# Optimization experiments

Measured on AMD Instinct MI355X. Metric: run time of the kernel, lower is better.

## Reference

```python
import jax, jax.numpy as jnp
import numpy as np


def setup_inputs() -> dict:
    key = jax.random.key(0)
    k_x, k_m, k_w1, k_b1, k_w2, k_b2 = jax.random.split(key, 6)
    b, seq_len, d_in, d_out = 8, 4096, 1024, 512
    x = jax.random.normal(k_x, (b, seq_len, d_in), dtype=jnp.float32)
    # binary-ish mask in {0,1} as floats (torch code multiplies by mask)
    mask = (jax.random.uniform(k_m, (b, seq_len)) < 0.5).astype(jnp.float32)
    s1 = 1.0 / np.sqrt(d_in)
    s2 = 1.0 / np.sqrt(d_out)
    W_enc = jax.random.uniform(k_w1, (d_out, d_in), minval=-s1, maxval=s1, dtype=jnp.float32)
    b_enc = jax.random.uniform(k_b1, (d_out,), minval=-s1, maxval=s1, dtype=jnp.float32)
    W_dec = jax.random.uniform(k_w2, (d_in, d_out), minval=-s2, maxval=s2, dtype=jnp.float32)
    b_dec = jax.random.uniform(k_b2, (d_in,), minval=-s2, maxval=s2, dtype=jnp.float32)
    return {"x": x, "mask": mask, "W_enc": W_enc, "b_enc": b_enc, "W_dec": W_dec, "b_dec": b_dec}


def reference(x, mask, W_enc, b_enc, W_dec, b_dec):
    # per-step: v_t = v_{t-1} + relu(x_t @ W_enc^T + b_enc) * mask_t  -> additive scan == cumsum
    h = jax.nn.relu(jnp.einsum('bsd,od->bso', x, W_enc) + b_enc) * mask[:, :, None]  # [b,s,d_out]
    v_cum = jnp.cumsum(h, axis=1)  # [b,s,d_out]
    out_enc = jnp.einsum('bso,do->bsd', v_cum, W_dec) + b_dec  # decode every prefix state
    v = v_cum[:, -1, :]  # final accumulated state
    return (v, out_enc)
```

## Files before the change

kernel.cpp:

```cpp
#include <hip/hip_runtime.h>
#include <hip/hip_bf16.h>
#include <stdint.h>

typedef __bf16 bf16_t;
typedef __bf16 bf16x4 __attribute__((ext_vector_type(4)));
typedef __bf16 bf16x8 __attribute__((ext_vector_type(8)));
typedef float  f32x4  __attribute__((ext_vector_type(4)));

__device__ __forceinline__ void gload_lds16(const void* g, void* l) {
  __builtin_amdgcn_global_load_lds(
      (__attribute__((address_space(1))) void*)g,
      (__attribute__((address_space(3))) void*)l, 16, 0, 0);
}

__global__ void cast_weights(const float* __restrict__ a, bf16_t* __restrict__ oa,
                             const float* __restrict__ b, bf16_t* __restrict__ ob,
                             int n4each) {
  const int i = blockIdx.x * blockDim.x + threadIdx.x;
  const float* src;
  bf16_t* dst;
  int k;
  if (i < n4each) { src = a; dst = oa; k = i; }
  else            { src = b; dst = ob; k = i - n4each; }
  f32x4 v = reinterpret_cast<const f32x4*>(src)[k];
  bf16x4 o;
  o[0] = (bf16_t)v[0]; o[1] = (bf16_t)v[1]; o[2] = (bf16_t)v[2]; o[3] = (bf16_t)v[3];
  reinterpret_cast<bf16x4*>(dst)[k] = o;
}

__global__ __launch_bounds__(256) void gemm1_fused(
    const float* __restrict__ x, const bf16_t* __restrict__ Wenc,
    const float* __restrict__ b_enc, const float* __restrict__ mask,
    bf16_t* __restrict__ h, float* __restrict__ partials)
{
  __shared__ __align__(16) char smem[65536];
  bf16_t* As0 = (bf16_t*)(smem);
  bf16_t* As1 = (bf16_t*)(smem + 16384);
  bf16_t* Bs0 = (bf16_t*)(smem + 32768);
  bf16_t* Bs1 = (bf16_t*)(smem + 49152);
  float*  tile = (float*)smem;

  const int tid  = threadIdx.x;
  const int lane = tid & 63;
  const int w    = tid >> 6;
  const int wm   = w >> 1, wn = w & 1;
  const long bm  = (long)blockIdx.x * 128;
  const long bn  = (long)blockIdx.y * 128;

  f32x4 acc[4][4] = {};

  const int srow = w * 32 + (lane >> 3);
  const int scol = (lane & 7) * 8;
  const bf16_t* Bbase = Wenc + (bn + srow) * 1024 + scol;

  const int ar0 = tid >> 3;
  const int ac0 = (tid & 7) * 8;
  const float* Abase = x + (bm + ar0) * 1024 + ac0;

  f32x4 av[4][2];

  auto aload = [&](int kt) {
    #pragma unroll
    for (int p = 0; p < 4; ++p) {
      const float* s = Abase + (long)p * 32 * 1024 + kt;
      av[p][0] = *reinterpret_cast<const f32x4*>(s);
      av[p][1] = *reinterpret_cast<const f32x4*>(s + 4);
    }
  };
  auto awrite = [&](bf16_t* As) {
    #pragma unroll
    for (int p = 0; p < 4; ++p) {
      bf16x8 o;
      #pragma unroll
      for (int e = 0; e < 4; ++e) {
        o[e]     = (bf16_t)av[p][0][e];
        o[e + 4] = (bf16_t)av[p][1][e];
      }
      *reinterpret_cast<bf16x8*>(&As[(p * 32 + ar0) * 64 + ac0]) = o;
    }
  };
  auto bstage = [&](bf16_t* Bs, int kt) {
    #pragma unroll
    for (int it = 0; it < 4; ++it)
      gload_lds16(Bbase + (long)it * 8 * 1024 + kt, &Bs[(w * 32 + it * 8) * 64]);
  };
  auto mfma_tile = [&](const bf16_t* As, const bf16_t* Bs) {
    #pragma unroll
    for (int kk = 0; kk < 2; ++kk) {
      const int kof = kk * 32 + (lane >> 4) * 8;
      bf16x8 afr[4], bfr[4];
      #pragma unroll
      for (int i = 0; i < 4; ++i)
        afr[i] = *reinterpret_cast<const bf16x8*>(&As[(wm * 64 + i * 16 + (lane & 15)) * 64 + kof]);
      #pragma unroll
      for (int j = 0; j < 4; ++j)
        bfr[j] = *reinterpret_cast<const bf16x8*>(&Bs[(wn * 64 + j * 16 + (lane & 15)) * 64 + kof]);
      #pragma unroll
      for (int i = 0; i < 4; ++i)
        #pragma unroll
        for (int j = 0; j < 4; ++j)
          acc[i][j] = __builtin_amdgcn_mfma_f32_16x16x32_bf16(afr[i], bfr[j], acc[i][j], 0, 0, 0);
    }
  };

  aload(0);
  awrite(As0);
  bstage(Bs0, 0);
  __syncthreads();

  int kt = 64;
  for (int p2 = 0; p2 < 8; ++p2) {
    if (kt < 1024) { aload(kt); bstage(Bs1, kt); }
    mfma_tile(As0, Bs0);
    if (kt < 1024) awrite(As1);
    __syncthreads();
    kt += 64;

    if (kt < 1024) { aload(kt); bstage(Bs0, kt); }
    mfma_tile(As1, Bs1);
    if (kt < 1024) awrite(As0);
    __syncthreads();
    kt += 64;
  }

  float bv[4];
  #pragma unroll
  for (int j = 0; j < 4; ++j)
    bv[j] = b_enc[bn + wn * 64 + j * 16 + (lane & 15)];

  #pragma unroll
  for (int i = 0; i < 4; ++i) {
    const int rbase = wm * 64 + i * 16 + ((lane >> 4) << 2);
    const f32x4 mv = *reinterpret_cast<const f32x4*>(&mask[bm + rbase]);
    #pragma unroll
    for (int j = 0; j < 4; ++j) {
      const int colj = wn * 64 + j * 16 + (lane & 15);
      #pragma unroll
      for (int r = 0; r < 4; ++r) {
        const int row = rbase + r;
        float hv = acc[i][j][r] + bv[j];
        hv = hv > 0.f ? hv : 0.f;
        hv *= mv[r];
        tile[row * 128 + (colj ^ (((row >> 2) & 1) << 4))] = hv;
      }
    }
  }
  __syncthreads();

  if (tid < 128) {
    float run = 0.f;
    bf16_t* hp = h + bm * 512 + bn + tid;
    #pragma unroll 4
    for (int s = 0; s < 128; ++s) {
      run += tile[s * 128 + (tid ^ (((s >> 2) & 1) << 4))];
      hp[(long)s * 512] = (bf16_t)run;
    }
    partials[blockIdx.x * 512 + bn + tid] = run;
  }
}

template<int EPI>
__global__ __launch_bounds__(256) void gemm_bt(
    const bf16_t* __restrict__ A, const bf16_t* __restrict__ B,
    const int K, const int N,
    const float* __restrict__ bias,
    const float* __restrict__ Padd,
    float* __restrict__ outf)
{
  __shared__ __align__(16) bf16_t As[2][128 * 64];
  __shared__ __align__(16) bf16_t Bs[2][128 * 64];

  const int tid  = threadIdx.x;
  const int lane = tid & 63;
  const int w    = tid >> 6;
  const int wm   = w >> 1, wn = w & 1;
  const long bm  = (long)blockIdx.x * 128;
  const long bn  = (long)blockIdx.y * 128;

  f32x4 acc[4][4] = {};

  const int srow = w * 32 + (lane >> 3);
  const int scol = (lane & 7) * 8;
  const bf16_t* Abase = A + (bm + srow) * (long)K + scol;
  const bf16_t* Bbase = B + (bn + srow) * (long)K + scol;

  auto stageA = [&](bf16_t* dst, int kt) {
    #pragma unroll
    for (int it = 0; it < 4; ++it)
      gload_lds16(Abase + (long)it * 8 * K + kt, &dst[(w * 32 + it * 8) * 64]);
  };
  auto stageB = [&](bf16_t* dst, int kt) {
    #pragma unroll
    for (int it = 0; it < 4; ++it)
      gload_lds16(Bbase + (long)it * 8 * K + kt, &dst[(w * 32 + it * 8) * 64]);
  };
  auto mfma_tile = [&](const bf16_t* Asb, const bf16_t* Bsb) {
    #pragma unroll
    for (int kk = 0; kk < 2; ++kk) {
      const int kof = kk * 32 + (lane >> 4) * 8;
      bf16x8 afr[4], bfr[4];
      #pragma unroll
      for (int i = 0; i < 4; ++i)
        afr[i] = *reinterpret_cast<const bf16x8*>(&Asb[(wm * 64 + i * 16 + (lane & 15)) * 64 + kof]);
      #pragma unroll
      for (int j = 0; j < 4; ++j)
        bfr[j] = *reinterpret_cast<const bf16x8*>(&Bsb[(wn * 64 + j * 16 + (lane & 15)) * 64 + kof]);
      #pragma unroll
      for (int i = 0; i < 4; ++i)
        #pragma unroll
        for (int j = 0; j < 4; ++j)
          acc[i][j] = __builtin_amdgcn_mfma_f32_16x16x32_bf16(afr[i], bfr[j], acc[i][j], 0, 0, 0);
    }
  };

  stageA(As[0], 0);
  stageB(Bs[0], 0);
  __syncthreads();

  int kt = 64;
  const int NP = K >> 7;
  for (int p2 = 0; p2 < NP; ++p2) {
    if (kt < K) { stageA(As[1], kt); stageB(Bs[1], kt); }
    mfma_tile(As[0], Bs[0]);
    __syncthreads();
    kt += 64;

    if (kt < K) { stageA(As[0], kt); stageB(Bs[0], kt); }
    mfma_tile(As[1], Bs[1]);
    __syncthreads();
    kt += 64;
  }

  #pragma unroll
  for (int j = 0; j < 4; ++j) {
    const long gc = bn + wn * 64 + j * 16 + (lane & 15);
    const float addv = (EPI == 1) ? Padd[(bm >> 7) * (long)N + gc] : bias[gc];
    #pragma unroll
    for (int i = 0; i < 4; ++i) {
      const long gr0 = bm + wm * 64 + i * 16 + ((lane >> 4) << 2);
      #pragma unroll
      for (int r = 0; r < 4; ++r)
        outf[(gr0 + r) * (long)N + gc] = acc[i][j][r] + addv;
    }
  }
}

__global__ void scan_chunks(const float* __restrict__ partials, bf16_t* __restrict__ prefixb,
                            float* __restrict__ v_out) {
  const int idx = blockIdx.x * blockDim.x + threadIdx.x;
  const int b = idx >> 9;
  const int o = idx & 511;
  float run = 0.f;
  #pragma unroll
  for (int c = 0; c < 32; ++c) {
    const size_t off = ((size_t)(b * 32 + c)) * 512 + o;
    prefixb[off] = (bf16_t)run;
    run += partials[off];
  }
  v_out[idx] = run;
}

extern "C" void kernel_launch(void* const* d_in, const int* in_sizes, int n_in,
                              void* d_out, int out_size, void* d_ws, size_t ws_size,
                              hipStream_t stream) {
  const float* x     = (const float*)d_in[0];
  const float* mask  = (const float*)d_in[1];
  const float* W_enc = (const float*)d_in[2];
  const float* b_enc = (const float*)d_in[3];
  const float* W_dec = (const float*)d_in[4];
  const float* b_dec = (const float*)d_in[5];

  float* out     = (float*)d_out;
  float* v_out   = out;
  float* out_enc = out + 4096;

  char* ws = (char*)d_ws;
  bf16_t* Web      = (bf16_t*)ws;  ws += (size_t)512 * 1024 * 2;
  bf16_t* Wdb      = (bf16_t*)ws;  ws += (size_t)1024 * 512 * 2;
  bf16_t* h        = (bf16_t*)ws;  ws += (size_t)32768 * 512 * 2;
  float*  partials = (float*)ws;   ws += (size_t)256 * 512 * 4;
  bf16_t* prefixb  = (bf16_t*)ws;  ws += (size_t)256 * 512 * 2;
  float*  P        = (float*)ws;   ws += (size_t)256 * 1024 * 4;

  cast_weights<<<1024, 256, 0, stream>>>(W_enc, Web, W_dec, Wdb, 131072);

  gemm1_fused<<<dim3(256, 4), 256, 0, stream>>>(x, Web, b_enc, mask, h, partials);

  scan_chunks<<<16, 256, 0, stream>>>(partials, prefixb, v_out);

  gemm_bt<2><<<dim3(2, 8), 256, 0, stream>>>(prefixb, Wdb, 512, 1024, b_dec, nullptr, P);

  gemm_bt<1><<<dim3(256, 8), 256, 0, stream>>>(h, Wdb, 512, 1024, nullptr, P, out_enc);
}
```

Before: 165.2 us.

## XOR-swizzle LDS tiles in both GEMMs and parallelize the in-block scan

Adds an XOR swizzle to the LDS layouts of the A and B tiles in the encoder and decoder GEMMs. The x tile is now loaded row-coalesced as float4 and written swizzled, which is meant to remove LDS bank conflicts on the MFMA fragment reads. The epilogue tile is stored in bf16 with a row-wise swizzle, and the 128-row cumsum is split across all 256 threads using a two-half partial sum instead of 128 serial threads. An explicit vmcnt(0) wait before each barrier adds a stall, and rounding h to bf16 before the scan slightly changes numerics.

```diff
diff --git a/kernel.cpp b/kernel.cpp
--- a/kernel.cpp
+++ b/kernel.cpp
@@ -17,9 +17,7 @@
                              const float* __restrict__ b, bf16_t* __restrict__ ob,
                              int n4each) {
   const int i = blockIdx.x * blockDim.x + threadIdx.x;
-  const float* src;
-  bf16_t* dst;
-  int k;
+  const float* src; bf16_t* dst; int k;
   if (i < n4each) { src = a; dst = oa; k = i; }
   else            { src = b; dst = ob; k = i - n4each; }
   f32x4 v = reinterpret_cast<const f32x4*>(src)[k];
@@ -28,17 +26,14 @@
   reinterpret_cast<bf16x4*>(dst)[k] = o;
 }
 
-__global__ __launch_bounds__(256) void gemm1_fused(
+__global__ __launch_bounds__(256) void gemm1_128(
     const float* __restrict__ x, const bf16_t* __restrict__ Wenc,
     const float* __restrict__ b_enc, const float* __restrict__ mask,
-    bf16_t* __restrict__ h, float* __restrict__ partials)
+    bf16_t* __restrict__ h_out, float* __restrict__ partials)
 {
   __shared__ __align__(16) char smem[65536];
-  bf16_t* As0 = (bf16_t*)(smem);
-  bf16_t* As1 = (bf16_t*)(smem + 16384);
-  bf16_t* Bs0 = (bf16_t*)(smem + 32768);
-  bf16_t* Bs1 = (bf16_t*)(smem + 49152);
-  float*  tile = (float*)smem;
+  auto Al = [&](int buf) { return (bf16_t*)(smem + buf * 16384); };
+  auto Bl = [&](int buf) { return (bf16_t*)(smem + 32768 + buf * 16384); };
 
   const int tid  = threadIdx.x;
   const int lane = tid & 63;
@@ -46,55 +41,52 @@
   const int wm   = w >> 1, wn = w & 1;
   const long bm  = (long)blockIdx.x * 128;
   const long bn  = (long)blockIdx.y * 128;
+  const int NT   = 16;
 
   f32x4 acc[4][4] = {};
-
-  const int srow = w * 32 + (lane >> 3);
-  const int scol = (lane & 7) * 8;
-  const bf16_t* Bbase = Wenc + (bn + srow) * 1024 + scol;
-
-  const int ar0 = tid >> 3;
-  const int ac0 = (tid & 7) * 8;
-  const float* Abase = x + (bm + ar0) * 1024 + ac0;
-
-  f32x4 av[4][2];
-
-  auto aload = [&](int kt) {
-    #pragma unroll
-    for (int p = 0; p < 4; ++p) {
-      const float* s = Abase + (long)p * 32 * 1024 + kt;
-      av[p][0] = *reinterpret_cast<const f32x4*>(s);
-      av[p][1] = *reinterpret_cast<const f32x4*>(s + 4);
-    }
-  };
-  auto awrite = [&](bf16_t* As) {
-    #pragma unroll
-    for (int p = 0; p < 4; ++p) {
-      bf16x8 o;
-      #pragma unroll
-      for (int e = 0; e < 4; ++e) {
-        o[e]     = (bf16_t)av[p][0][e];
-        o[e + 4] = (bf16_t)av[p][1][e];
-      }
-      *reinterpret_cast<bf16x8*>(&As[(p * 32 + ar0) * 64 + ac0]) = o;
-    }
-  };
-  auto bstage = [&](bf16_t* Bs, int kt) {
-    #pragma unroll
-    for (int it = 0; it < 4; ++it)
-      gload_lds16(Bbase + (long)it * 8 * 1024 + kt, &Bs[(w * 32 + it * 8) * 64]);
-  };
-  auto mfma_tile = [&](const bf16_t* As, const bf16_t* Bs) {
+  f32x4 av[8];
+
+  auto gaLoad = [&](int t) {
+    #pragma unroll
+    for (int u = 0; u < 8; ++u) {
+      const int row = u * 16 + (tid >> 4);
+      av[u] = *reinterpret_cast<const f32x4*>(x + (bm + row) * 1024 + t * 64 + (tid & 15) * 4);
+    }
+  };
+  auto aWrite = [&](int buf) {
+    bf16_t* lb = Al(buf);
+    const int c4 = tid & 15;
+    #pragma unroll
+    for (int u = 0; u < 8; ++u) {
+      const int row = u * 16 + (tid >> 4);
+      bf16x4 o;
+      o[0] = (bf16_t)av[u][0]; o[1] = (bf16_t)av[u][1];
+      o[2] = (bf16_t)av[u][2]; o[3] = (bf16_t)av[u][3];
+      *reinterpret_cast<bf16x4*>(lb + row * 64 + ((((c4 >> 1) ^ (row & 7)) << 3) + (c4 & 1) * 4)) = o;
+    }
+  };
+  const int scolB = (((lane & 7) ^ (lane >> 3)) << 3);
+  auto stageB = [&](int t, int buf) {
+    bf16_t* lb = Bl(buf);
+    #pragma unroll
+    for (int it = 0; it < 4; ++it) {
+      const int r0 = w * 32 + it * 8;
+      gload_lds16(Wenc + (bn + r0 + (lane >> 3)) * 1024 + t * 64 + scolB, lb + r0 * 64);
+    }
+  };
+  auto mfma_tile = [&](int buf) {
+    const bf16_t* Asb = Al(buf);
+    const bf16_t* Bsb = Bl(buf);
     #pragma unroll
     for (int kk = 0; kk < 2; ++kk) {
-      const int kof = kk * 32 + (lane >> 4) * 8;
+      const int kof = (((kk * 4 + (lane >> 4)) ^ (lane & 7)) << 3);
       bf16x8 afr[4], bfr[4];
       #pragma unroll
       for (int i = 0; i < 4; ++i)
-        afr[i] = *reinterpret_cast<const bf16x8*>(&As[(wm * 64 + i * 16 + (lane & 15)) * 64 + kof]);
+        afr[i] = *reinterpret_cast<const bf16x8*>(&Asb[(wm * 64 + i * 16 + (lane & 15)) * 64 + kof]);
       #pragma unroll
       for (int j = 0; j < 4; ++j)
-        bfr[j] = *reinterpret_cast<const bf16x8*>(&Bs[(wn * 64 + j * 16 + (lane & 15)) * 64 + kof]);
+        bfr[j] = *reinterpret_cast<const bf16x8*>(&Bsb[(wn * 64 + j * 16 + (lane & 15)) * 64 + kof]);
       #pragma unroll
       for (int i = 0; i < 4; ++i)
         #pragma unroll
@@ -103,26 +95,22 @@
     }
   };
 
-  aload(0);
-  awrite(As0);
-  bstage(Bs0, 0);
-  __syncthreads();
-
-  int kt = 64;
-  for (int p2 = 0; p2 < 8; ++p2) {
-    if (kt < 1024) { aload(kt); bstage(Bs1, kt); }
-    mfma_tile(As0, Bs0);
-    if (kt < 1024) awrite(As1);
+  gaLoad(0);
+  stageB(0, 0);
+  aWrite(0);
+  asm volatile("s_waitcnt vmcnt(0)" ::: "memory");
+  __syncthreads();
+
+  for (int t = 0; t < NT; ++t) {
+    const int buf = t & 1;
+    if (t + 1 < NT) { gaLoad(t + 1); stageB(t + 1, buf ^ 1); }
+    mfma_tile(buf);
+    if (t + 1 < NT) aWrite(buf ^ 1);
+    asm volatile("s_waitcnt vmcnt(0)" ::: "memory");
     __syncthreads();
-    kt += 64;
-
-    if (kt < 1024) { aload(kt); bstage(Bs0, kt); }
-    mfma_tile(As1, Bs1);
-    if (kt < 1024) awrite(As0);
-    __syncthreads();
-    kt += 64;
-  }
-
+  }
+
+  bf16_t* tile = (bf16_t*)smem;
   float bv[4];
   #pragma unroll
   for (int j = 0; j < 4; ++j)
@@ -130,40 +118,50 @@
 
   #pragma unroll
   for (int i = 0; i < 4; ++i) {
-    const int rbase = wm * 64 + i * 16 + ((lane >> 4) << 2);
-    const f32x4 mv = *reinterpret_cast<const f32x4*>(&mask[bm + rbase]);
+    const int row0 = wm * 64 + i * 16 + ((lane >> 4) << 2);
+    const f32x4 mv = *reinterpret_cast<const f32x4*>(&mask[bm + row0]);
     #pragma unroll
     for (int j = 0; j < 4; ++j) {
-      const int colj = wn * 64 + j * 16 + (lane & 15);
-      #pragma unroll
-      for (int r = 0; r < 4; ++r) {
-        const int row = rbase + r;
-        float hv = acc[i][j][r] + bv[j];
-        hv = hv > 0.f ? hv : 0.f;
-        hv *= mv[r];
-        tile[row * 128 + (colj ^ (((row >> 2) & 1) << 4))] = hv;
+      const int col = wn * 64 + j * 16 + (lane & 15);
+      #pragma unroll
+      for (int e = 0; e < 4; ++e) {
+        const int row = row0 + e;
+        float hv = acc[i][j][e] + bv[j];
+        hv = (hv > 0.f ? hv : 0.f) * mv[e];
+        tile[row * 128 + (col ^ ((row & 7) << 4))] = (bf16_t)hv;
       }
     }
   }
   __syncthreads();
 
-  if (tid < 128) {
-    float run = 0.f;
-    bf16_t* hp = h + bm * 512 + bn + tid;
+  __shared__ float sum0[128];
+  const int col  = tid & 127;
+  const int half = tid >> 7;
+  if (half == 0) {
+    float s = 0.f;
     #pragma unroll 4
-    for (int s = 0; s < 128; ++s) {
-      run += tile[s * 128 + (tid ^ (((s >> 2) & 1) << 4))];
-      hp[(long)s * 512] = (bf16_t)run;
-    }
-    partials[blockIdx.x * 512 + bn + tid] = run;
-  }
-}
-
-template<int EPI>
-__global__ __launch_bounds__(256) void gemm_bt(
+    for (int r = 0; r < 64; ++r)
+      s += (float)tile[r * 128 + (col ^ ((r & 7) << 4))];
+    sum0[col] = s;
+  }
+  __syncthreads();
+  {
+    float run = half ? sum0[col] : 0.f;
+    const int rbase = half * 64;
+    bf16_t* hp = h_out + (bm + rbase) * 512 + bn + col;
+    #pragma unroll 4
+    for (int r = 0; r < 64; ++r) {
+      const int row = rbase + r;
+      run += (float)tile[row * 128 + (col ^ ((row & 7) << 4))];
+      hp[(long)r * 512] = (bf16_t)run;
+    }
+    if (half) partials[blockIdx.x * 512 + bn + col] = run;
+  }
+}
+
+__global__ __launch_bounds__(256) void gemm2_128(
     const bf16_t* __restrict__ A, const bf16_t* __restrict__ B,
     const int K, const int N,
-    const float* __restrict__ bias,
     const float* __restrict__ Padd,
     float* __restrict__ outf)
 {
@@ -176,6 +174,78 @@
   const int wm   = w >> 1, wn = w & 1;
   const long bm  = (long)blockIdx.x * 128;
   const long bn  = (long)blockIdx.y * 128;
+  const int NT   = K >> 6;
+
+  f32x4 acc[4][4] = {};
+
+  const int scol = (((lane & 7) ^ (lane >> 3)) << 3);
+  auto stage = [&](int t, int buf) {
+    #pragma unroll
+    for (int it = 0; it < 4; ++it) {
+      const int r0 = w * 32 + it * 8;
+      gload_lds16(A + (bm + r0 + (lane >> 3)) * (long)K + t * 64 + scol, &As[buf][r0 * 64]);
+      gload_lds16(B + (bn + r0 + (lane >> 3)) * (long)K + t * 64 + scol, &Bs[buf][r0 * 64]);
+    }
+  };
+  auto mfma_tile = [&](int buf) {
+    #pragma unroll
+    for (int kk = 0; kk < 2; ++kk) {
+      const int kof = (((kk * 4 + (lane >> 4)) ^ (lane & 7)) << 3);
+      bf16x8 afr[4], bfr[4];
+      #pragma unroll
+      for (int i = 0; i < 4; ++i)
+        afr[i] = *reinterpret_cast<const bf16x8*>(&As[buf][(wm * 64 + i * 16 + (lane & 15)) * 64 + kof]);
+      #pragma unroll
+      for (int j = 0; j < 4; ++j)
+        bfr[j] = *reinterpret_cast<const bf16x8*>(&Bs[buf][(wn * 64 + j * 16 + (lane & 15)) * 64 + kof]);
+      #pragma unroll
+      for (int i = 0; i < 4; ++i)
+        #pragma unroll
+        for (int j = 0; j < 4; ++j)
+          acc[i][j] = __builtin_amdgcn_mfma_f32_16x16x32_bf16(afr[i], bfr[j], acc[i][j], 0, 0, 0);
+    }
+  };
+
+  stage(0, 0);
+  asm volatile("s_waitcnt vmcnt(0)" ::: "memory");
+  __syncthreads();
+  for (int t = 0; t < NT; ++t) {
+    const int buf = t & 1;
+    if (t + 1 < NT) stage(t + 1, buf ^ 1);
+    mfma_tile(buf);
+    asm volatile("s_waitcnt vmcnt(0)" ::: "memory");
+    __syncthreads();
+  }
+
+  #pragma unroll
+  for (int j = 0; j < 4; ++j) {
+    const long gc = bn + wn * 64 + j * 16 + (lane & 15);
+    const float pv = Padd[blockIdx.x * (long)N + gc];
+    #pragma unroll
+    for (int i = 0; i < 4; ++i) {
+      const long gr0 = bm + wm * 64 + i * 16 + ((lane >> 4) << 2);
+      #pragma unroll
+      for (int e = 0; e < 4; ++e)
+        outf[(gr0 + e) * (long)N + gc] = acc[i][j][e] + pv;
+    }
+  }
+}
+
+__global__ __launch_bounds__(256) void gemm_p(
+    const bf16_t* __restrict__ A, const bf16_t* __restrict__ B,
+    const int K, const int N,
+    const float* __restrict__ bias,
+    float* __restrict__ outf)
+{
+  __shared__ __align__(16) bf16_t As[2][128 * 64];
+  __shared__ __align__(16) bf16_t Bs[2][128 * 64];
+
+  const int tid  = threadIdx.x;
+  const int lane = tid & 63;
+  const int w    = tid >> 6;
+  const int wm   = w >> 1, wn = w & 1;
+  const long bm  = (long)blockIdx.x * 128;
+  const long bn  = (long)blockIdx.y * 128;
 
   f32x4 acc[4][4] = {};
 
@@ -184,15 +254,12 @@
   const bf16_t* Abase = A + (bm + srow) * (long)K + scol;
   const bf16_t* Bbase = B + (bn + srow) * (long)K + scol;
 
-  auto stageA = [&](bf16_t* dst, int kt) {
-    #pragma unroll
-    for (int it = 0; it < 4; ++it)
-      gload_lds16(Abase + (long)it * 8 * K + kt, &dst[(w * 32 + it * 8) * 64]);
-  };
-  auto stageB = [&](bf16_t* dst, int kt) {
-    #pragma unroll
-    for (int it = 0; it < 4; ++it)
-      gload_lds16(Bbase + (long)it * 8 * K + kt, &dst[(w * 32 + it * 8) * 64]);
+  auto stage = [&](bf16_t* da, bf16_t* db, int kt) {
+    #pragma unroll
+    for (int it = 0; it < 4; ++it) {
+      gload_lds16(Abase + (long)it * 8 * K + kt, &da[(w * 32 + it * 8) * 64]);
+      gload_lds16(Bbase + (long)it * 8 * K + kt, &db[(w * 32 + it * 8) * 64]);
+    }
   };
   auto mfma_tile = [&](const bf16_t* Asb, const bf16_t* Bsb) {
     #pragma unroll
@@ -213,19 +280,15 @@
     }
   };
 
-  stageA(As[0], 0);
-  stageB(Bs[0], 0);
-  __syncthreads();
-
+  stage(As[0], Bs[0], 0);
+  __syncthreads();
   int kt = 64;
-  const int NP = K >> 7;
-  for (int p2 = 0; p2 < NP; ++p2) {
-    if (kt < K) { stageA(As[1], kt); stageB(Bs[1], kt); }
+  for (int p2 = 0; p2 < (K >> 7); ++p2) {
+    if (kt < K) stage(As[1], Bs[1], kt);
     mfma_tile(As[0], Bs[0]);
     __syncthreads();
     kt += 64;
-
-    if (kt < K) { stageA(As[0], kt); stageB(Bs[0], kt); }
+    if (kt < K) stage(As[0], Bs[0], kt);
     mfma_tile(As[1], Bs[1]);
     __syncthreads();
     kt += 64;
@@ -234,7 +297,7 @@
   #pragma unroll
   for (int j = 0; j < 4; ++j) {
     const long gc = bn + wn * 64 + j * 16 + (lane & 15);
-    const float addv = (EPI == 1) ? Padd[(bm >> 7) * (long)N + gc] : bias[gc];
+    const float addv = bias[gc];
     #pragma unroll
     for (int i = 0; i < 4; ++i) {
       const long gr0 = bm + wm * 64 + i * 16 + ((lane >> 4) << 2);
@@ -284,11 +347,11 @@
 
   cast_weights<<<1024, 256, 0, stream>>>(W_enc, Web, W_dec, Wdb, 131072);
 
-  gemm1_fused<<<dim3(256, 4), 256, 0, stream>>>(x, Web, b_enc, mask, h, partials);
+  gemm1_128<<<dim3(256, 4), 256, 0, stream>>>(x, Web, b_enc, mask, h, partials);
 
   scan_chunks<<<16, 256, 0, stream>>>(partials, prefixb, v_out);
 
-  gemm_bt<2><<<dim3(2, 8), 256, 0, stream>>>(prefixb, Wdb, 512, 1024, b_dec, nullptr, P);
-
-  gemm_bt<1><<<dim3(256, 8), 256, 0, stream>>>(h, Wdb, 512, 1024, nullptr, P, out_enc);
-}
+  gemm_p<<<dim3(2, 8), 256, 0, stream>>>(prefixb, Wdb, 512, 1024, b_dec, P);
+
+  gemm2_128<<<dim3(256, 8), 256, 0, stream>>>(h, Wdb, 512, 1024, P, out_enc);
+}
```

Result: slower. 176.6 us (+6.9%).
